# Optimization experiments

Measured on AMD Instinct MI355X. Metric: run time of the kernel, lower is better.

## Reference

```python
import jax, jax.numpy as jnp
import numpy as np

B = 64          # batches
T = 65536       # total packed tokens
X = 512         # token feature dim
K = 5           # io pairs
Y = X * K       # extra dim = 2560
H = 512         # hidden


def setup_inputs() -> dict:
    key = jax.random.key(0)
    ks = jax.random.split(key, 13)
    s = 0.02  # weight scale
    return {
        "ps_data": jax.random.normal(ks[0], (T, X), jnp.float32),
        "io_embed": jax.random.normal(ks[1], (B, K, X), jnp.float32),
        "segment_ids": jnp.sort(jax.random.randint(ks[2], (T,), 0, B, dtype=jnp.int32)),
        # attention_fc: Linear(X+Y,512) -> ReLU -> Linear(512,512) -> ReLU -> Linear(512,1)
        "W1": jax.random.normal(ks[3], (X + Y, H), jnp.float32) * s,
        "b1": jnp.zeros((H,), jnp.float32),
        "W2": jax.random.normal(ks[4], (H, H), jnp.float32) * s,
        "b2": jnp.zeros((H,), jnp.float32),
        "W3": jax.random.normal(ks[5], (H, 1), jnp.float32) * s,
        "b3": jnp.zeros((1,), jnp.float32),
        # final_fc: Linear(512,512) -> ReLU -> Linear(512,2)
        "Wf1": jax.random.normal(ks[6], (H, H), jnp.float32) * s,
        "bf1": jnp.zeros((H,), jnp.float32),
        "Wf2": jax.random.normal(ks[7], (H, 2), jnp.float32) * s,
        "bf2": jnp.zeros((2,), jnp.float32),
    }


def reference(ps_data, io_embed, segment_ids, W1, b1, W2, b2, W3, b3, Wf1, bf1, Wf2, bf2):
    # io_embed (B,K,X) -> (B,Y); gather per token by its batch index
    extra = io_embed.reshape(B, -1)[segment_ids]            # (T, Y)
    h = jnp.concatenate([ps_data, extra], axis=1)           # (T, X+Y)
    h = jax.nn.relu(h @ W1 + b1)
    h = jax.nn.relu(h @ W2 + b2)
    logits = (h @ W3 + b3)[:, 0]                            # (T,)
    # per-segment softmax over ragged segments
    m = jax.lax.stop_gradient(
        jax.ops.segment_max(logits, segment_ids, num_segments=B))
    e = jnp.exp(logits - m[segment_ids])
    denom = jax.ops.segment_sum(e, segment_ids, num_segments=B)
    w = e / denom[segment_ids]                              # (T,)
    pooled = jax.ops.segment_sum(w[:, None] * ps_data, segment_ids,
                                 num_segments=B)            # (B, X)
    # final_fc
    return jax.nn.relu(pooled @ Wf1 + bf1) @ Wf2 + bf2      # (B, 2)
```

## Files before the change

### kernel.cpp

```cpp
#include <hip/hip_runtime.h>

#define T_TOK 65536
#define BATCH 64
#define XDIM  512
#define HDIM  512
#define YDIM  2560

#define TM 128
#define TN 128
#define BK 64

#define SB_KC 64
#define SB_KS 40
#define SB_BG 8

#define PREP_CONV   16384
#define PREP_TRANS  2048
#define PREP_SB     320

typedef float  f32x4  __attribute__((ext_vector_type(4)));
typedef __bf16 bf16x8 __attribute__((ext_vector_type(8)));

__device__ __forceinline__ unsigned short f2bf(float f) {
    unsigned int u = __float_as_uint(f);
    return (unsigned short)((u + 0x7FFFu + ((u >> 16) & 1u)) >> 16);
}

__device__ __forceinline__ float bf2f(unsigned short u) {
    return __uint_as_float((unsigned int)u << 16);
}

__device__ __forceinline__ void load_lds16(const unsigned short* g, unsigned short* l) {
    __builtin_amdgcn_global_load_lds(
        (const __attribute__((address_space(1))) unsigned int*)g,
        (__attribute__((address_space(3))) unsigned int*)l, 16, 0, 0);
}

__device__ __forceinline__ int lower_bound_seg(const int* __restrict__ s, int n, int v) {
    int lo = 0, hi = n;
    while (lo < hi) { int mid = (lo + hi) >> 1; if (s[mid] < v) lo = mid + 1; else hi = mid; }
    return lo;
}

__global__ __launch_bounds__(256) void prep_kernel(const float* __restrict__ ps,
                                                   unsigned short* __restrict__ psb,
                                                   const float* __restrict__ W1,
                                                   const float* __restrict__ W2,
                                                   unsigned short* __restrict__ w1t,
                                                   unsigned short* __restrict__ w2t,
                                                   const float* __restrict__ io,
                                                   float* __restrict__ partial) {
    __shared__ float sio[SB_BG][SB_KC];
    const int blk = blockIdx.x;
    const int t = threadIdx.x;

    if (blk < PREP_CONV) {
        size_t idx = (size_t)blk * 256 + t;
        const float4* s4 = reinterpret_cast<const float4*>(ps) + idx * 2;
        float4 a = s4[0], b = s4[1];
        ushort4 o0, o1;
        o0.x = f2bf(a.x); o0.y = f2bf(a.y); o0.z = f2bf(a.z); o0.w = f2bf(a.w);
        o1.x = f2bf(b.x); o1.y = f2bf(b.y); o1.z = f2bf(b.z); o1.w = f2bf(b.w);
        reinterpret_cast<ushort4*>(psb)[idx * 2 + 0] = o0;
        reinterpret_cast<ushort4*>(psb)[idx * 2 + 1] = o1;
    } else if (blk < PREP_CONV + PREP_TRANS) {
        int bb = blk - PREP_CONV;
        const float* src = bb < 1024 ? W1 : W2;
        unsigned short* dst = bb < 1024 ? w1t : w2t;
        int idx = (bb & 1023) * 256 + t;
        int nn = idx >> 9, kk = idx & 511;
        dst[idx] = f2bf(src[(size_t)kk * 512 + nn]);
    } else {
        int sb = blk - PREP_CONV - PREP_TRANS;
        int s = sb >> 3, g = sb & 7;
        for (int i = t; i < SB_BG * SB_KC; i += 256) {
            int bb = i >> 6, kk = i & 63;
            sio[bb][kk] = io[(size_t)(g * SB_BG + bb) * YDIM + s * SB_KC + kk];
        }
        __syncthreads();
        float acc[SB_BG][2] = {};
        const int k0 = 512 + s * SB_KC;
        #pragma unroll 4
        for (int kk = 0; kk < SB_KC; kk++) {
            float wa = W1[(size_t)(k0 + kk) * 512 + t];
            float wb = W1[(size_t)(k0 + kk) * 512 + t + 256];
            #pragma unroll
            for (int bb = 0; bb < SB_BG; bb++) {
                acc[bb][0] += sio[bb][kk] * wa;
                acc[bb][1] += sio[bb][kk] * wb;
            }
        }
        #pragma unroll
        for (int bb = 0; bb < SB_BG; bb++) {
            int b = g * SB_BG + bb;
            partial[((size_t)s * BATCH + b) * 512 + t]       = acc[bb][0];
            partial[((size_t)s * BATCH + b) * 512 + t + 256] = acc[bb][1];
        }
    }
}

__global__ __launch_bounds__(256) void segbias_reduce(const float* __restrict__ partial,
                                                      float* __restrict__ segbias) {
    int idx = blockIdx.x * 256 + threadIdx.x;
    float s = 0.f;
    #pragma unroll
    for (int i = 0; i < SB_KS; i++) s += partial[(size_t)i * BATCH * 512 + idx];
    segbias[idx] = s;
}

#define STAGE_TILE(sh, src, row0, kt, rowlen)                                    \
    _Pragma("unroll")                                                            \
    for (int i_ = 0; i_ < 4; i_++) {                                             \
        int g_ = i_ * 256 + t;                                                   \
        int r_ = g_ >> 3, cs_ = g_ & 7;                                          \
        int csrc_ = cs_ ^ (r_ & 7);                                              \
        load_lds16(src + (size_t)(row0 + r_) * rowlen + kt + csrc_ * 8,          \
                   &sh[g_ * 8]);                                                 \
    }

#define FRAG_AT(sh, R, c) (*reinterpret_cast<const bf16x8*>(&sh[(((R) * 8) + ((c) ^ ((R) & 7))) * 8]))

__global__ __launch_bounds__(256) void gemm1_kernel(const unsigned short* __restrict__ psb,
                                                    const unsigned short* __restrict__ w1t,
                                                    const float* __restrict__ segbias,
                                                    const float* __restrict__ b1,
                                                    const int* __restrict__ segids,
                                                    unsigned short* __restrict__ h1) {
    __shared__ unsigned short shA[TM * BK];
    __shared__ unsigned short shB[TN * BK];

    const int bid = blockIdx.x;
    const int xcd = bid & 7;
    const int j = bid >> 3;
    const int n0 = (j & 3) * TN;
    const int m0 = ((j >> 2) * 8 + xcd) * TM;
    const int t = threadIdx.x;
    const int w = t >> 6, L = t & 63;
    const int mbase = (w >> 1) * 64, nbase = (w & 1) * 64;
    const int lrow = L & 15, lq = L >> 4;

    f32x4 acc[4][4] = {};

    for (int kt = 0; kt < XDIM; kt += BK) {
        STAGE_TILE(shA, psb, m0, kt, XDIM)
        STAGE_TILE(shB, w1t, n0, kt, HDIM)
        __syncthreads();
        #pragma unroll
        for (int ks = 0; ks < BK; ks += 32) {
            bf16x8 af[4], bfr[4];
            #pragma unroll
            for (int i = 0; i < 4; i++) {
                int R = mbase + i * 16 + lrow;
                af[i] = FRAG_AT(shA, R, (ks >> 3) + lq);
            }
            #pragma unroll
            for (int jj = 0; jj < 4; jj++) {
                int R = nbase + jj * 16 + lrow;
                bfr[jj] = FRAG_AT(shB, R, (ks >> 3) + lq);
            }
            #pragma unroll
            for (int i = 0; i < 4; i++)
                #pragma unroll
                for (int jj = 0; jj < 4; jj++)
                    acc[i][jj] = __builtin_amdgcn_mfma_f32_16x16x32_bf16(af[i], bfr[jj], acc[i][jj], 0, 0, 0);
        }
        __syncthreads();
    }

    #pragma unroll
    for (int i = 0; i < 4; i++) {
        #pragma unroll
        for (int r = 0; r < 4; r++) {
            int gm = m0 + mbase + i * 16 + lq * 4 + r;
            int sg = segids[gm];
            const float* sb = segbias + (size_t)sg * HDIM;
            #pragma unroll
            for (int jj = 0; jj < 4; jj++) {
                int gn = n0 + nbase + jj * 16 + lrow;
                float v = acc[i][jj][r] + sb[gn] + b1[gn];
                v = v > 0.f ? v : 0.f;
                h1[(size_t)gm * HDIM + gn] = f2bf(v);
            }
        }
    }
}

__global__ __launch_bounds__(256) void gemm2_kernel(const unsigned short* __restrict__ h1,
                                                    const unsigned short* __restrict__ w2t,
                                                    const float* __restrict__ b2,
                                                    const float* __restrict__ w3,
                                                    float* __restrict__ logits) {
    __shared__ unsigned short shA[TM * BK];
    __shared__ unsigned short shB[TN * BK];

    const int bid = blockIdx.x;
    const int xcd = bid & 7;
    const int j = bid >> 3;
    const int n0 = (j & 3) * TN;
    const int m0 = ((j >> 2) * 8 + xcd) * TM;
    const int t = threadIdx.x;
    const int w = t >> 6, L = t & 63;
    const int mbase = (w >> 1) * 64, nbase = (w & 1) * 64;
    const int lrow = L & 15, lq = L >> 4;

    f32x4 acc[4][4] = {};

    for (int kt = 0; kt < HDIM; kt += BK) {
        STAGE_TILE(shA, h1, m0, kt, HDIM)
        STAGE_TILE(shB, w2t, n0, kt, HDIM)
        __syncthreads();
        #pragma unroll
        for (int ks = 0; ks < BK; ks += 32) {
            bf16x8 af[4], bfr[4];
            #pragma unroll
            for (int i = 0; i < 4; i++) {
                int R = mbase + i * 16 + lrow;
                af[i] = FRAG_AT(shA, R, (ks >> 3) + lq);
            }
            #pragma unroll
            for (int jj = 0; jj < 4; jj++) {
                int R = nbase + jj * 16 + lrow;
                bfr[jj] = FRAG_AT(shB, R, (ks >> 3) + lq);
            }
            #pragma unroll
            for (int i = 0; i < 4; i++)
                #pragma unroll
                for (int jj = 0; jj < 4; jj++)
                    acc[i][jj] = __builtin_amdgcn_mfma_f32_16x16x32_bf16(af[i], bfr[jj], acc[i][jj], 0, 0, 0);
        }
        __syncthreads();
    }

    float w3v[4], b2v[4];
    #pragma unroll
    for (int jj = 0; jj < 4; jj++) {
        int gn = n0 + nbase + jj * 16 + lrow;
        w3v[jj] = w3[gn];
        b2v[jj] = b2[gn];
    }
    #pragma unroll
    for (int i = 0; i < 4; i++) {
        #pragma unroll
        for (int r = 0; r < 4; r++) {
            float p = 0.f;
            #pragma unroll
            for (int jj = 0; jj < 4; jj++) {
                float h2 = acc[i][jj][r] + b2v[jj];
                h2 = h2 > 0.f ? h2 : 0.f;
                p += h2 * w3v[jj];
            }
            p += __shfl_xor(p, 1, 64);
            p += __shfl_xor(p, 2, 64);
            p += __shfl_xor(p, 4, 64);
            p += __shfl_xor(p, 8, 64);
            if (lrow == 0)
                atomicAdd(&logits[m0 + mbase + i * 16 + lq * 4 + r], p);
        }
    }
}

__global__ __launch_bounds__(256) void stats_kernel(const float* __restrict__ logits,
                                                    const int* __restrict__ segids,
                                                    float* __restrict__ stats) {
    const int b = blockIdx.x;
    const int t = threadIdx.x;
    __shared__ float sred[4];
    const int start = lower_bound_seg(segids, T_TOK, b);
    const int end   = lower_bound_seg(segids, T_TOK, b + 1);
    float m = -3.4e38f;
    for (int i = start + t; i < end; i += 256) m = fmaxf(m, logits[i]);
    for (int d = 32; d; d >>= 1) m = fmaxf(m, __shfl_down(m, d, 64));
    if ((t & 63) == 0) sred[t >> 6] = m;
    __syncthreads();
    m = fmaxf(fmaxf(sred[0], sred[1]), fmaxf(sred[2], sred[3]));
    __syncthreads();
    float s = 0.f;
    for (int i = start + t; i < end; i += 256) s += __expf(logits[i] - m);
    for (int d = 32; d; d >>= 1) s += __shfl_down(s, d, 64);
    if ((t & 63) == 0) sred[t >> 6] = s;
    __syncthreads();
    if (t == 0) { stats[2 * b] = m; stats[2 * b + 1] = sred[0] + sred[1] + sred[2] + sred[3]; }
}

__global__ __launch_bounds__(512) void pool_kernel(const unsigned short* __restrict__ psb,
                                                   const float* __restrict__ logits,
                                                   const int* __restrict__ segids,
                                                   const float* __restrict__ stats,
                                                   float* __restrict__ pooled) {
    const int s = blockIdx.x;
    const int b = blockIdx.y;
    const int t = threadIdx.x;
    __shared__ float wv[512];
    const int start = lower_bound_seg(segids, T_TOK, b);
    const int end   = lower_bound_seg(segids, T_TOK, b + 1);
    const int n = end - start;
    const int per = (n + 15) >> 4;
    const int s0 = start + s * per;
    const int s1 = min(s0 + per, end);
    const float m = stats[2 * b];
    const float inv = 1.f / stats[2 * b + 1];
    float acc = 0.f;
    for (int base = s0; base < s1; base += 512) {
        int cnt = min(512, s1 - base);
        __syncthreads();
        if (t < cnt) wv[t] = __expf(logits[base + t] - m) * inv;
        __syncthreads();
        for (int i = 0; i < cnt; i++)
            acc += wv[i] * bf2f(psb[(size_t)(base + i) * XDIM + t]);
    }
    if (s1 > s0) atomicAdd(&pooled[b * XDIM + t], acc);
}

__global__ __launch_bounds__(512) void final_kernel(const float* __restrict__ pooled,
                                                    const float* __restrict__ wf1,
                                                    const float* __restrict__ bf1,
                                                    const float* __restrict__ wf2,
                                                    const float* __restrict__ bf2,
                                                    float* __restrict__ out) {
    const int b = blockIdx.x;
    const int t = threadIdx.x;
    __shared__ float sp[512];
    __shared__ float r0s[8], r1s[8];
    sp[t] = pooled[b * XDIM + t];
    __syncthreads();
    float acc = bf1[t];
    #pragma unroll 4
    for (int k = 0; k < 512; k++) acc += sp[k] * wf1[(size_t)k * 512 + t];
    float h = fmaxf(acc, 0.f);
    float p0 = h * wf2[t * 2 + 0];
    float p1 = h * wf2[t * 2 + 1];
    for (int d = 32; d; d >>= 1) { p0 += __shfl_down(p0, d, 64); p1 += __shfl_down(p1, d, 64); }
    if ((t & 63) == 0) { r0s[t >> 6] = p0; r1s[t >> 6] = p1; }
    __syncthreads();
    if (t == 0) {
        float a = 0.f, c = 0.f;
        #pragma unroll
        for (int i = 0; i < 8; i++) { a += r0s[i]; c += r1s[i]; }
        out[b * 2 + 0] = a + bf2[0];
        out[b * 2 + 1] = c + bf2[1];
    }
}

extern "C" void kernel_launch(void* const* d_in, const int* in_sizes, int n_in,
                              void* d_out, int out_size, void* d_ws, size_t ws_size,
                              hipStream_t stream) {
    const float* ps  = (const float*)d_in[0];
    const float* io  = (const float*)d_in[1];
    const int*   seg = (const int*)d_in[2];
    const float* W1  = (const float*)d_in[3];
    const float* b1  = (const float*)d_in[4];
    const float* W2  = (const float*)d_in[5];
    const float* b2  = (const float*)d_in[6];
    const float* W3  = (const float*)d_in[7];
    const float* Wf1 = (const float*)d_in[9];
    const float* bf1 = (const float*)d_in[10];
    const float* Wf2 = (const float*)d_in[11];
    const float* bf2 = (const float*)d_in[12];
    float* out = (float*)d_out;

    char* ws = (char*)d_ws;
    float*          segbias = (float*)(ws + 0);
    float*          logits  = (float*)(ws + 131072);
    float*          stats   = (float*)(ws + 393216);
    float*          pooled  = (float*)(ws + 397312);
    unsigned short* w1t     = (unsigned short*)(ws + 528384);
    unsigned short* w2t     = (unsigned short*)(ws + 1052672);
    unsigned short* h1      = (unsigned short*)(ws + 1576960);
    unsigned short* psb     = (unsigned short*)(ws + 68685824);
    float*          partial = (float*)(ws + 1576960);

    hipMemsetAsync(ws + 131072, 0, 262144, stream);
    hipMemsetAsync(ws + 397312, 0, 131072, stream);

    prep_kernel<<<PREP_CONV + PREP_TRANS + PREP_SB, 256, 0, stream>>>(
        ps, psb, W1, W2, w1t, w2t, io, partial);
    segbias_reduce<<<128, 256, 0, stream>>>(partial, segbias);
    gemm1_kernel<<<2048, 256, 0, stream>>>(psb, w1t, segbias, b1, seg, h1);
    gemm2_kernel<<<2048, 256, 0, stream>>>(h1, w2t, b2, W3, logits);
    stats_kernel<<<64, 256, 0, stream>>>(logits, seg, stats);
    pool_kernel<<<dim3(16, 64), 512, 0, stream>>>(psb, logits, seg, stats, pooled);
    final_kernel<<<64, 512, 0, stream>>>(pooled, Wf1, bf1, Wf2, bf2, out);
}
```

Baseline: 424.6 us.

## Fuse both hidden-layer GEMMs into one kernel keeping h1 tile in LDS

Replaces the separate gemm1 and gemm2 kernels with a single kernel that computes a 32-row h1 tile into shared memory and then immediately runs the second GEMM and W3 projection on it. This removes the global round trip of the bf16 h1 activation, the logits memset and the atomic adds. In exchange each block uses a much smaller M tile, so W1 and W2 are re-streamed from L2 by every block and each wave does far fewer MFMAs per LDS fragment load, lowering arithmetic intensity.

```diff
diff --git a/kernel.cpp b/kernel.cpp
--- a/kernel.cpp
+++ b/kernel.cpp
@@ -6,9 +6,8 @@
 #define HDIM  512
 #define YDIM  2560
 
-#define TM 128
-#define TN 128
 #define BK 64
+#define FTM 32
 
 #define SB_KC 64
 #define SB_KS 40
@@ -108,155 +107,133 @@
     segbias[idx] = s;
 }
 
-#define STAGE_TILE(sh, src, row0, kt, rowlen)                                    \
-    _Pragma("unroll")                                                            \
-    for (int i_ = 0; i_ < 4; i_++) {                                             \
-        int g_ = i_ * 256 + t;                                                   \
-        int r_ = g_ >> 3, cs_ = g_ & 7;                                          \
-        int csrc_ = cs_ ^ (r_ & 7);                                              \
-        load_lds16(src + (size_t)(row0 + r_) * rowlen + kt + csrc_ * 8,          \
-                   &sh[g_ * 8]);                                                 \
-    }
-
-#define FRAG_AT(sh, R, c) (*reinterpret_cast<const bf16x8*>(&sh[(((R) * 8) + ((c) ^ ((R) & 7))) * 8]))
-
-__global__ __launch_bounds__(256) void gemm1_kernel(const unsigned short* __restrict__ psb,
-                                                    const unsigned short* __restrict__ w1t,
-                                                    const float* __restrict__ segbias,
-                                                    const float* __restrict__ b1,
-                                                    const int* __restrict__ segids,
-                                                    unsigned short* __restrict__ h1) {
-    __shared__ unsigned short shA[TM * BK];
-    __shared__ unsigned short shB[TN * BK];
-
-    const int bid = blockIdx.x;
-    const int xcd = bid & 7;
-    const int j = bid >> 3;
-    const int n0 = (j & 3) * TN;
-    const int m0 = ((j >> 2) * 8 + xcd) * TM;
+#define FRAG8(sh, R, c)  (*reinterpret_cast<const bf16x8*>(&(sh)[((R) * 8  + (((c) ^ ((R) & 7)))) * 8]))
+#define FRAG64(sh, R, c) (*reinterpret_cast<const bf16x8*>(&(sh)[((R) * 64 + (((c) ^ ((R) & 7)))) * 8]))
+
+__global__ __launch_bounds__(256) void fused_gemm(const unsigned short* __restrict__ psb,
+                                                  const unsigned short* __restrict__ w1t,
+                                                  const unsigned short* __restrict__ w2t,
+                                                  const float* __restrict__ segbias,
+                                                  const float* __restrict__ b1,
+                                                  const float* __restrict__ b2,
+                                                  const float* __restrict__ w3,
+                                                  const int* __restrict__ segids,
+                                                  float* __restrict__ logits) {
+    __shared__ unsigned short h1t[FTM * 512];
+    __shared__ unsigned short shA[FTM * BK];
+    __shared__ unsigned short shB[128 * BK];
+    __shared__ float part[FTM][4];
+
+    const int m0 = blockIdx.x * FTM;
     const int t = threadIdx.x;
     const int w = t >> 6, L = t & 63;
-    const int mbase = (w >> 1) * 64, nbase = (w & 1) * 64;
     const int lrow = L & 15, lq = L >> 4;
-
-    f32x4 acc[4][4] = {};
-
-    for (int kt = 0; kt < XDIM; kt += BK) {
-        STAGE_TILE(shA, psb, m0, kt, XDIM)
-        STAGE_TILE(shB, w1t, n0, kt, HDIM)
-        __syncthreads();
-        #pragma unroll
-        for (int ks = 0; ks < BK; ks += 32) {
-            bf16x8 af[4], bfr[4];
-            #pragma unroll
-            for (int i = 0; i < 4; i++) {
-                int R = mbase + i * 16 + lrow;
-                af[i] = FRAG_AT(shA, R, (ks >> 3) + lq);
-            }
-            #pragma unroll
-            for (int jj = 0; jj < 4; jj++) {
-                int R = nbase + jj * 16 + lrow;
-                bfr[jj] = FRAG_AT(shB, R, (ks >> 3) + lq);
-            }
-            #pragma unroll
-            for (int i = 0; i < 4; i++)
-                #pragma unroll
-                for (int jj = 0; jj < 4; jj++)
-                    acc[i][jj] = __builtin_amdgcn_mfma_f32_16x16x32_bf16(af[i], bfr[jj], acc[i][jj], 0, 0, 0);
-        }
-        __syncthreads();
-    }
-
-    #pragma unroll
-    for (int i = 0; i < 4; i++) {
-        #pragma unroll
-        for (int r = 0; r < 4; r++) {
-            int gm = m0 + mbase + i * 16 + lq * 4 + r;
-            int sg = segids[gm];
-            const float* sb = segbias + (size_t)sg * HDIM;
-            #pragma unroll
-            for (int jj = 0; jj < 4; jj++) {
-                int gn = n0 + nbase + jj * 16 + lrow;
-                float v = acc[i][jj][r] + sb[gn] + b1[gn];
-                v = v > 0.f ? v : 0.f;
-                h1[(size_t)gm * HDIM + gn] = f2bf(v);
-            }
-        }
-    }
-}
-
-__global__ __launch_bounds__(256) void gemm2_kernel(const unsigned short* __restrict__ h1,
-                                                    const unsigned short* __restrict__ w2t,
-                                                    const float* __restrict__ b2,
-                                                    const float* __restrict__ w3,
-                                                    float* __restrict__ logits) {
-    __shared__ unsigned short shA[TM * BK];
-    __shared__ unsigned short shB[TN * BK];
-
-    const int bid = blockIdx.x;
-    const int xcd = bid & 7;
-    const int j = bid >> 3;
-    const int n0 = (j & 3) * TN;
-    const int m0 = ((j >> 2) * 8 + xcd) * TM;
-    const int t = threadIdx.x;
-    const int w = t >> 6, L = t & 63;
-    const int mbase = (w >> 1) * 64, nbase = (w & 1) * 64;
-    const int lrow = L & 15, lq = L >> 4;
-
-    f32x4 acc[4][4] = {};
-
-    for (int kt = 0; kt < HDIM; kt += BK) {
-        STAGE_TILE(shA, h1, m0, kt, HDIM)
-        STAGE_TILE(shB, w2t, n0, kt, HDIM)
-        __syncthreads();
-        #pragma unroll
-        for (int ks = 0; ks < BK; ks += 32) {
-            bf16x8 af[4], bfr[4];
-            #pragma unroll
-            for (int i = 0; i < 4; i++) {
-                int R = mbase + i * 16 + lrow;
-                af[i] = FRAG_AT(shA, R, (ks >> 3) + lq);
-            }
-            #pragma unroll
-            for (int jj = 0; jj < 4; jj++) {
-                int R = nbase + jj * 16 + lrow;
-                bfr[jj] = FRAG_AT(shB, R, (ks >> 3) + lq);
-            }
-            #pragma unroll
-            for (int i = 0; i < 4; i++)
-                #pragma unroll
-                for (int jj = 0; jj < 4; jj++)
-                    acc[i][jj] = __builtin_amdgcn_mfma_f32_16x16x32_bf16(af[i], bfr[jj], acc[i][jj], 0, 0, 0);
-        }
-        __syncthreads();
-    }
-
-    float w3v[4], b2v[4];
-    #pragma unroll
-    for (int jj = 0; jj < 4; jj++) {
-        int gn = n0 + nbase + jj * 16 + lrow;
-        w3v[jj] = w3[gn];
-        b2v[jj] = b2[gn];
-    }
-    #pragma unroll
-    for (int i = 0; i < 4; i++) {
-        #pragma unroll
-        for (int r = 0; r < 4; r++) {
-            float p = 0.f;
-            #pragma unroll
-            for (int jj = 0; jj < 4; jj++) {
-                float h2 = acc[i][jj][r] + b2v[jj];
-                h2 = h2 > 0.f ? h2 : 0.f;
-                p += h2 * w3v[jj];
-            }
-            p += __shfl_xor(p, 1, 64);
-            p += __shfl_xor(p, 2, 64);
-            p += __shfl_xor(p, 4, 64);
-            p += __shfl_xor(p, 8, 64);
-            if (lrow == 0)
-                atomicAdd(&logits[m0 + mbase + i * 16 + lq * 4 + r], p);
-        }
-    }
+    const int ncol = w * 32;
+
+    for (int ns = 0; ns < 4; ns++) {
+        f32x4 acc[2][2] = {};
+        for (int kt = 0; kt < XDIM; kt += BK) {
+            {
+                int r_ = t >> 3, c_ = t & 7, cs_ = c_ ^ (r_ & 7);
+                load_lds16(psb + (size_t)(m0 + r_) * XDIM + kt + cs_ * 8, &shA[t * 8]);
+            }
+            #pragma unroll
+            for (int i_ = 0; i_ < 4; i_++) {
+                int g_ = i_ * 256 + t;
+                int r_ = g_ >> 3, c_ = g_ & 7, cs_ = c_ ^ (r_ & 7);
+                load_lds16(w1t + (size_t)(ns * 128 + r_) * HDIM + kt + cs_ * 8, &shB[g_ * 8]);
+            }
+            __syncthreads();
+            #pragma unroll
+            for (int ks = 0; ks < BK; ks += 32) {
+                bf16x8 af[2], bf[2];
+                #pragma unroll
+                for (int i = 0; i < 2; i++) af[i] = FRAG8(shA, i * 16 + lrow, (ks >> 3) + lq);
+                #pragma unroll
+                for (int j = 0; j < 2; j++) bf[j] = FRAG8(shB, ncol + j * 16 + lrow, (ks >> 3) + lq);
+                #pragma unroll
+                for (int i = 0; i < 2; i++)
+                    #pragma unroll
+                    for (int j = 0; j < 2; j++)
+                        acc[i][j] = __builtin_amdgcn_mfma_f32_16x16x32_bf16(af[i], bf[j], acc[i][j], 0, 0, 0);
+            }
+            __syncthreads();
+        }
+        #pragma unroll
+        for (int i = 0; i < 2; i++) {
+            #pragma unroll
+            for (int r = 0; r < 4; r++) {
+                int hr = i * 16 + lq * 4 + r;
+                int sg = segids[m0 + hr];
+                const float* sb = segbias + (size_t)sg * HDIM;
+                #pragma unroll
+                for (int j = 0; j < 2; j++) {
+                    int hc = ns * 128 + ncol + j * 16 + lrow;
+                    float v = acc[i][j][r] + sb[hc] + b1[hc];
+                    v = v > 0.f ? v : 0.f;
+                    h1t[hr * 512 + (((hc >> 3) ^ (hr & 7)) * 8) + (hc & 7)] = f2bf(v);
+                }
+            }
+        }
+    }
+    __syncthreads();
+
+    float lp[2][4] = {};
+    for (int ns2 = 0; ns2 < 4; ns2++) {
+        f32x4 acc[2][2] = {};
+        for (int kt = 0; kt < HDIM; kt += BK) {
+            #pragma unroll
+            for (int i_ = 0; i_ < 4; i_++) {
+                int g_ = i_ * 256 + t;
+                int r_ = g_ >> 3, c_ = g_ & 7, cs_ = c_ ^ (r_ & 7);
+                load_lds16(w2t + (size_t)(ns2 * 128 + r_) * HDIM + kt + cs_ * 8, &shB[g_ * 8]);
+            }
+            __syncthreads();
+            #pragma unroll
+            for (int ks = 0; ks < BK; ks += 32) {
+                bf16x8 af[2], bf[2];
+                #pragma unroll
+                for (int i = 0; i < 2; i++) af[i] = FRAG64(h1t, i * 16 + lrow, ((kt + ks) >> 3) + lq);
+                #pragma unroll
+                for (int j = 0; j < 2; j++) bf[j] = FRAG8(shB, ncol + j * 16 + lrow, (ks >> 3) + lq);
+                #pragma unroll
+                for (int i = 0; i < 2; i++)
+                    #pragma unroll
+                    for (int j = 0; j < 2; j++)
+                        acc[i][j] = __builtin_amdgcn_mfma_f32_16x16x32_bf16(af[i], bf[j], acc[i][j], 0, 0, 0);
+            }
+            __syncthreads();
+        }
+        #pragma unroll
+        for (int i = 0; i < 2; i++) {
+            #pragma unroll
+            for (int r = 0; r < 4; r++) {
+                float p = 0.f;
+                #pragma unroll
+                for (int j = 0; j < 2; j++) {
+                    int gn = ns2 * 128 + ncol + j * 16 + lrow;
+                    float h2 = acc[i][j][r] + b2[gn];
+                    h2 = h2 > 0.f ? h2 : 0.f;
+                    p += h2 * w3[gn];
+                }
+                p += __shfl_xor(p, 1, 64);
+                p += __shfl_xor(p, 2, 64);
+                p += __shfl_xor(p, 4, 64);
+                p += __shfl_xor(p, 8, 64);
+                lp[i][r] += p;
+            }
+        }
+    }
+    if (lrow == 0) {
+        #pragma unroll
+        for (int i = 0; i < 2; i++)
+            #pragma unroll
+            for (int r = 0; r < 4; r++)
+                part[i * 16 + lq * 4 + r][w] = lp[i][r];
+    }
+    __syncthreads();
+    if (t < FTM)
+        logits[m0 + t] = part[t][0] + part[t][1] + part[t][2] + part[t][3];
 }
 
 __global__ __launch_bounds__(256) void stats_kernel(const float* __restrict__ logits,
@@ -365,18 +342,15 @@
     float*          pooled  = (float*)(ws + 397312);
     unsigned short* w1t     = (unsigned short*)(ws + 528384);
     unsigned short* w2t     = (unsigned short*)(ws + 1052672);
-    unsigned short* h1      = (unsigned short*)(ws + 1576960);
-    unsigned short* psb     = (unsigned short*)(ws + 68685824);
     float*          partial = (float*)(ws + 1576960);
-
-    hipMemsetAsync(ws + 131072, 0, 262144, stream);
+    unsigned short* psb     = (unsigned short*)(ws + 8388608);
+
     hipMemsetAsync(ws + 397312, 0, 131072, stream);
 
     prep_kernel<<<PREP_CONV + PREP_TRANS + PREP_SB, 256, 0, stream>>>(
         ps, psb, W1, W2, w1t, w2t, io, partial);
     segbias_reduce<<<128, 256, 0, stream>>>(partial, segbias);
-    gemm1_kernel<<<2048, 256, 0, stream>>>(psb, w1t, segbias, b1, seg, h1);
-    gemm2_kernel<<<2048, 256, 0, stream>>>(h1, w2t, b2, W3, logits);
+    fused_gemm<<<T_TOK / FTM, 256, 0, stream>>>(psb, w1t, w2t, segbias, b1, b2, W3, seg, logits);
     stats_kernel<<<64, 256, 0, stream>>>(logits, seg, stats);
     pool_kernel<<<dim3(16, 64), 512, 0, stream>>>(psb, logits, seg, stats, pooled);
     final_kernel<<<64, 512, 0, stream>>>(pooled, Wf1, bf1, Wf2, bf2, out);
```

Measured after the change: 453.4 us. 6.8% more time.

## Use 256x128 GEMM tiles with 512 threads and replace logit atomics with slice partials

Applied to the files above, without the earlier changes.

Both GEMM kernels move to 256x128 output tiles with 512-thread blocks (8 waves, each still computing 64x64), which halves the number of blocks and reloads of the weight tile. Gemm2 now writes each per-slice partial logit to its own slot in an 8-slice buffer instead of using atomicAdd. The stats kernel sums those slices and writes the final logits, which also removes the memset of the logits buffer. The workspace layout is rearranged to fit the larger buffers, and the larger block uses more LDS per workgroup.

```diff
diff --git a/kernel.cpp b/kernel.cpp
--- a/kernel.cpp
+++ b/kernel.cpp
@@ -6,9 +6,9 @@
 #define HDIM  512
 #define YDIM  2560
 
-#define TM 128
-#define TN 128
 #define BK 64
+#define GM_TM 256
+#define GM_TN 128
 
 #define SB_KC 64
 #define SB_KS 40
@@ -108,32 +108,22 @@
     segbias[idx] = s;
 }
 
-#define STAGE_TILE(sh, src, row0, kt, rowlen)                                    \
-    _Pragma("unroll")                                                            \
-    for (int i_ = 0; i_ < 4; i_++) {                                             \
-        int g_ = i_ * 256 + t;                                                   \
-        int r_ = g_ >> 3, cs_ = g_ & 7;                                          \
-        int csrc_ = cs_ ^ (r_ & 7);                                              \
-        load_lds16(src + (size_t)(row0 + r_) * rowlen + kt + csrc_ * 8,          \
-                   &sh[g_ * 8]);                                                 \
-    }
-
-#define FRAG_AT(sh, R, c) (*reinterpret_cast<const bf16x8*>(&sh[(((R) * 8) + ((c) ^ ((R) & 7))) * 8]))
-
-__global__ __launch_bounds__(256) void gemm1_kernel(const unsigned short* __restrict__ psb,
+#define FRAG_AT(sh, R, c) (*reinterpret_cast<const bf16x8*>(&(sh)[((R) * 8 + (((c) ^ ((R) & 7)))) * 8]))
+
+__global__ __launch_bounds__(512) void gemm1_kernel(const unsigned short* __restrict__ psb,
                                                     const unsigned short* __restrict__ w1t,
                                                     const float* __restrict__ segbias,
                                                     const float* __restrict__ b1,
                                                     const int* __restrict__ segids,
                                                     unsigned short* __restrict__ h1) {
-    __shared__ unsigned short shA[TM * BK];
-    __shared__ unsigned short shB[TN * BK];
+    __shared__ unsigned short shA[GM_TM * BK];
+    __shared__ unsigned short shB[GM_TN * BK];
 
     const int bid = blockIdx.x;
     const int xcd = bid & 7;
     const int j = bid >> 3;
-    const int n0 = (j & 3) * TN;
-    const int m0 = ((j >> 2) * 8 + xcd) * TM;
+    const int n0 = (j & 3) * GM_TN;
+    const int m0 = ((j >> 2) * 8 + xcd) * GM_TM;
     const int t = threadIdx.x;
     const int w = t >> 6, L = t & 63;
     const int mbase = (w >> 1) * 64, nbase = (w & 1) * 64;
@@ -142,22 +132,26 @@
     f32x4 acc[4][4] = {};
 
     for (int kt = 0; kt < XDIM; kt += BK) {
-        STAGE_TILE(shA, psb, m0, kt, XDIM)
-        STAGE_TILE(shB, w1t, n0, kt, HDIM)
+        #pragma unroll
+        for (int i_ = 0; i_ < 4; i_++) {
+            int g_ = i_ * 512 + t;
+            int r_ = g_ >> 3, c_ = g_ & 7, cs_ = c_ ^ (r_ & 7);
+            load_lds16(psb + (size_t)(m0 + r_) * XDIM + kt + cs_ * 8, &shA[g_ * 8]);
+        }
+        #pragma unroll
+        for (int i_ = 0; i_ < 2; i_++) {
+            int g_ = i_ * 512 + t;
+            int r_ = g_ >> 3, c_ = g_ & 7, cs_ = c_ ^ (r_ & 7);
+            load_lds16(w1t + (size_t)(n0 + r_) * HDIM + kt + cs_ * 8, &shB[g_ * 8]);
+        }
         __syncthreads();
         #pragma unroll
         for (int ks = 0; ks < BK; ks += 32) {
             bf16x8 af[4], bfr[4];
             #pragma unroll
-            for (int i = 0; i < 4; i++) {
-                int R = mbase + i * 16 + lrow;
-                af[i] = FRAG_AT(shA, R, (ks >> 3) + lq);
-            }
-            #pragma unroll
-            for (int jj = 0; jj < 4; jj++) {
-                int R = nbase + jj * 16 + lrow;
-                bfr[jj] = FRAG_AT(shB, R, (ks >> 3) + lq);
-            }
+            for (int i = 0; i < 4; i++) af[i] = FRAG_AT(shA, mbase + i * 16 + lrow, (ks >> 3) + lq);
+            #pragma unroll
+            for (int jj = 0; jj < 4; jj++) bfr[jj] = FRAG_AT(shB, nbase + jj * 16 + lrow, (ks >> 3) + lq);
             #pragma unroll
             for (int i = 0; i < 4; i++)
                 #pragma unroll
@@ -185,19 +179,19 @@
     }
 }
 
-__global__ __launch_bounds__(256) void gemm2_kernel(const unsigned short* __restrict__ h1,
+__global__ __launch_bounds__(512) void gemm2_kernel(const unsigned short* __restrict__ h1,
                                                     const unsigned short* __restrict__ w2t,
                                                     const float* __restrict__ b2,
                                                     const float* __restrict__ w3,
-                                                    float* __restrict__ logits) {
-    __shared__ unsigned short shA[TM * BK];
-    __shared__ unsigned short shB[TN * BK];
+                                                    float* __restrict__ logits8) {
+    __shared__ unsigned short shA[GM_TM * BK];
+    __shared__ unsigned short shB[GM_TN * BK];
 
     const int bid = blockIdx.x;
     const int xcd = bid & 7;
     const int j = bid >> 3;
-    const int n0 = (j & 3) * TN;
-    const int m0 = ((j >> 2) * 8 + xcd) * TM;
+    const int n0 = (j & 3) * GM_TN;
+    const int m0 = ((j >> 2) * 8 + xcd) * GM_TM;
     const int t = threadIdx.x;
     const int w = t >> 6, L = t & 63;
     const int mbase = (w >> 1) * 64, nbase = (w & 1) * 64;
@@ -206,22 +200,26 @@
     f32x4 acc[4][4] = {};
 
     for (int kt = 0; kt < HDIM; kt += BK) {
-        STAGE_TILE(shA, h1, m0, kt, HDIM)
-        STAGE_TILE(shB, w2t, n0, kt, HDIM)
+        #pragma unroll
+        for (int i_ = 0; i_ < 4; i_++) {
+            int g_ = i_ * 512 + t;
+            int r_ = g_ >> 3, c_ = g_ & 7, cs_ = c_ ^ (r_ & 7);
+            load_lds16(h1 + (size_t)(m0 + r_) * HDIM + kt + cs_ * 8, &shA[g_ * 8]);
+        }
+        #pragma unroll
+        for (int i_ = 0; i_ < 2; i_++) {
+            int g_ = i_ * 512 + t;
+            int r_ = g_ >> 3, c_ = g_ & 7, cs_ = c_ ^ (r_ & 7);
+            load_lds16(w2t + (size_t)(n0 + r_) * HDIM + kt + cs_ * 8, &shB[g_ * 8]);
+        }
         __syncthreads();
         #pragma unroll
         for (int ks = 0; ks < BK; ks += 32) {
             bf16x8 af[4], bfr[4];
             #pragma unroll
-            for (int i = 0; i < 4; i++) {
-                int R = mbase + i * 16 + lrow;
-                af[i] = FRAG_AT(shA, R, (ks >> 3) + lq);
-            }
-            #pragma unroll
-            for (int jj = 0; jj < 4; jj++) {
-                int R = nbase + jj * 16 + lrow;
-                bfr[jj] = FRAG_AT(shB, R, (ks >> 3) + lq);
-            }
+            for (int i = 0; i < 4; i++) af[i] = FRAG_AT(shA, mbase + i * 16 + lrow, (ks >> 3) + lq);
+            #pragma unroll
+            for (int jj = 0; jj < 4; jj++) bfr[jj] = FRAG_AT(shB, nbase + jj * 16 + lrow, (ks >> 3) + lq);
             #pragma unroll
             for (int i = 0; i < 4; i++)
                 #pragma unroll
@@ -238,6 +236,7 @@
         w3v[jj] = w3[gn];
         b2v[jj] = b2[gn];
     }
+    const int slice = (j & 3) * 2 + (w & 1);
     #pragma unroll
     for (int i = 0; i < 4; i++) {
         #pragma unroll
@@ -254,12 +253,13 @@
             p += __shfl_xor(p, 4, 64);
             p += __shfl_xor(p, 8, 64);
             if (lrow == 0)
-                atomicAdd(&logits[m0 + mbase + i * 16 + lq * 4 + r], p);
-        }
-    }
-}
-
-__global__ __launch_bounds__(256) void stats_kernel(const float* __restrict__ logits,
+                logits8[(size_t)slice * T_TOK + m0 + mbase + i * 16 + lq * 4 + r] = p;
+        }
+    }
+}
+
+__global__ __launch_bounds__(256) void stats_kernel(const float* __restrict__ logits8,
+                                                    float* __restrict__ logits,
                                                     const int* __restrict__ segids,
                                                     float* __restrict__ stats) {
     const int b = blockIdx.x;
@@ -268,7 +268,13 @@
     const int start = lower_bound_seg(segids, T_TOK, b);
     const int end   = lower_bound_seg(segids, T_TOK, b + 1);
     float m = -3.4e38f;
-    for (int i = start + t; i < end; i += 256) m = fmaxf(m, logits[i]);
+    for (int i = start + t; i < end; i += 256) {
+        float l = 0.f;
+        #pragma unroll
+        for (int s = 0; s < 8; s++) l += logits8[(size_t)s * T_TOK + i];
+        logits[i] = l;
+        m = fmaxf(m, l);
+    }
     for (int d = 32; d; d >>= 1) m = fmaxf(m, __shfl_down(m, d, 64));
     if ((t & 63) == 0) sred[t >> 6] = m;
     __syncthreads();
@@ -365,19 +371,19 @@
     float*          pooled  = (float*)(ws + 397312);
     unsigned short* w1t     = (unsigned short*)(ws + 528384);
     unsigned short* w2t     = (unsigned short*)(ws + 1052672);
-    unsigned short* h1      = (unsigned short*)(ws + 1576960);
-    unsigned short* psb     = (unsigned short*)(ws + 68685824);
-    float*          partial = (float*)(ws + 1576960);
-
-    hipMemsetAsync(ws + 131072, 0, 262144, stream);
+    float*          logits8 = (float*)(ws + 1576960);
+    float*          partial = (float*)(ws + 3674112);
+    unsigned short* psb     = (unsigned short*)(ws + 16777216);
+    unsigned short* h1      = (unsigned short*)(ws + 83886080);
+
     hipMemsetAsync(ws + 397312, 0, 131072, stream);
 
     prep_kernel<<<PREP_CONV + PREP_TRANS + PREP_SB, 256, 0, stream>>>(
         ps, psb, W1, W2, w1t, w2t, io, partial);
     segbias_reduce<<<128, 256, 0, stream>>>(partial, segbias);
-    gemm1_kernel<<<2048, 256, 0, stream>>>(psb, w1t, segbias, b1, seg, h1);
-    gemm2_kernel<<<2048, 256, 0, stream>>>(h1, w2t, b2, W3, logits);
-    stats_kernel<<<64, 256, 0, stream>>>(logits, seg, stats);
+    gemm1_kernel<<<(T_TOK / GM_TM) * 4, 512, 0, stream>>>(psb, w1t, segbias, b1, seg, h1);
+    gemm2_kernel<<<(T_TOK / GM_TM) * 4, 512, 0, stream>>>(h1, w2t, b2, W3, logits8);
+    stats_kernel<<<64, 256, 0, stream>>>(logits8, logits, seg, stats);
     pool_kernel<<<dim3(16, 64), 512, 0, stream>>>(psb, logits, seg, stats, pooled);
     final_kernel<<<64, 512, 0, stream>>>(pooled, Wf1, bf1, Wf2, bf2, out);
 }
```

New measurement: 391.7 us. 1.08x faster.
